# Kernel optimization log

Measured on AMD Instinct MI355X. Metric: run time of the kernel, lower is better.

The kernel has to match this reference:

```python
import jax, jax.numpy as jnp
import numpy as np

# Static per-expert capacities (tokens are laid out contiguously per expert)
CAPS = [1024, 512, 1024, 256, 1024, 512, 128, 1024, 512, 1024, 256, 512, 1024, 128, 64, 512]
TOTAL = sum(CAPS)  # 9536
E, H, I = 16, 1024, 4096
OFFSETS = np.concatenate([[0], np.cumsum(CAPS)])


def setup_inputs() -> dict:
    key = jax.random.key(0)
    ks = jax.random.split(key, 5)
    x = jax.random.normal(ks[0], (TOTAL, H), dtype=jnp.float32)
    W1 = jax.random.normal(ks[1], (E, I, H), dtype=jnp.float32) * 0.02
    b1 = jax.random.normal(ks[2], (E, I), dtype=jnp.float32) * 0.02
    W2 = jax.random.normal(ks[3], (E, H, I), dtype=jnp.float32) * 0.02
    b2 = jax.random.normal(ks[4], (E, H), dtype=jnp.float32) * 0.02
    return {"x": x, "W1": W1, "b1": b1, "W2": W2, "b2": b2}


def reference(x, W1, b1, W2, b2):
    # Grouped GEMM FFN: expert e processes rows [OFFSETS[e]:OFFSETS[e+1]]
    # out = gelu(x_e @ W1[e].T + b1[e]) @ W2[e].T + b2[e]
    outs = []
    for e in range(E):  # fixed, static loop over experts (capacities are static)
        xs = x[OFFSETS[e]:OFFSETS[e + 1]]                      # [cap_e, H]
        h = jax.nn.gelu(xs @ W1[e].T + b1[e], approximate=False)  # [cap_e, I]
        outs.append(h @ W2[e].T + b2[e])                       # [cap_e, H]
    return jnp.concatenate(outs, axis=0)                       # [TOTAL, H]
```

## Files before the change

### kernel.cpp

```cpp
#include <hip/hip_runtime.h>
#include <math.h>

typedef __attribute__((ext_vector_type(8))) short short8;
typedef __attribute__((ext_vector_type(4))) float f32x4;
typedef __attribute__((ext_vector_type(2))) unsigned int u32x2;
typedef __attribute__((ext_vector_type(4))) unsigned int u32x4;

#define E_NUM 16
constexpr int CAPS[E_NUM] = {1024,512,1024,256,1024,512,128,1024,512,1024,256,512,1024,128,64,512};
constexpr int OFFS[E_NUM] = {0,1024,1536,2560,2816,3840,4352,4480,5504,6016,7040,7296,7808,8832,8960,9024};
constexpr int cdiv_(int a, int b){ return (a + b - 1) / b; }
constexpr int ilog2_(int v){ int l = 0; while ((1 << l) < v) ++l; return l; }

__device__ __forceinline__ unsigned int cvt_pk_bf16(float a, float b){
  unsigned int r;
  asm("v_cvt_pk_bf16_f32 %0, %1, %2" : "=v"(r) : "v"(a), "v"(b));
  return r;
}

typedef __attribute__((address_space(1))) const unsigned char gas_u8;
typedef __attribute__((address_space(3))) unsigned char las_u8;
__device__ __forceinline__ void gl_lds16(const void* g, void* l){
  __builtin_amdgcn_global_load_lds((gas_u8*)g, (las_u8*)l, 16, 0, 0);
}

__global__ __launch_bounds__(256) void cvt_bf16_kernel(const float* __restrict__ x,
                                                       unsigned short* __restrict__ xb, int n8)
{
  int i = blockIdx.x * blockDim.x + threadIdx.x;
  const int stride = gridDim.x * blockDim.x;
  for (; i < n8; i += stride) {
    f32x4 a = *reinterpret_cast<const f32x4*>(x + (size_t)i * 8);
    f32x4 b = *reinterpret_cast<const f32x4*>(x + (size_t)i * 8 + 4);
    u32x2 lo, hi;
    lo[0] = cvt_pk_bf16(a[0], a[1]); lo[1] = cvt_pk_bf16(a[2], a[3]);
    hi[0] = cvt_pk_bf16(b[0], b[1]); hi[1] = cvt_pk_bf16(b[2], b[3]);
    *reinterpret_cast<u32x2*>(xb + (size_t)i * 8)     = lo;
    *reinterpret_cast<u32x2*>(xb + (size_t)i * 8 + 4) = hi;
  }
}

template<bool A_BF16, int NDIM, int KDIM, int LOG_GN, int NWG>
__global__ __launch_bounds__(512, 2)
void g1_gemm256(const void* __restrict__ Av, const float* __restrict__ W,
                const float* __restrict__ bias, void* __restrict__ Outv)
{
  constexpr int A_BYTES = 256 * 64;
  constexpr int B_BYTES = 256 * 128;
  constexpr int BUF  = A_BYTES + B_BYTES;
  constexpr int NBUF = A_BF16 ? 3 : 2;
  constexpr int GN   = 1 << LOG_GN;
  constexpr int NTT  = KDIM / 32;
  static_assert(NWG % 8 == 0);
  static_assert(NTT >= 3);

  __shared__ __align__(16) char smem[NBUF * BUF];

  const int tid  = threadIdx.x;
  const int braw = blockIdx.x;
  const int tt = (braw & 7) * (NWG / 8) + (braw >> 3);

  int m0 = 0, n0 = 0, Me = 0, tok0 = 0;
  size_t wbase = 0, bbase = 0;
  {
    int acc0 = 0;
    #pragma unroll
    for (int i = 0; i < E_NUM; ++i) {
      const int mt  = cdiv_(CAPS[i], 256);
      const int lmt = ilog2_(mt);
      const int nb  = mt * (NDIM / 256);
      if (tt >= acc0 && tt < acc0 + nb) {
        const int loc = tt - acc0;
        const int g   = loc >> (lmt + LOG_GN);
        const int rem = loc & ((mt << LOG_GN) - 1);
        m0   = (rem >> LOG_GN) * 256;
        n0   = ((g << LOG_GN) | (rem & (GN - 1))) * 256;
        Me   = CAPS[i];
        tok0 = OFFS[i];
        wbase = (size_t)i * NDIM * KDIM;
        bbase = (size_t)i * NDIM;
      }
      acc0 += nb;
    }
  }
  const float* Wb = W + wbase;

  const int lane = tid & 63;
  const int wv   = tid >> 6;

  const unsigned short* Ah = (const unsigned short*)Av;
  const float*          Af = (const float*)Av;

  auto stageA = [&](int buf, int kt) {
    const unsigned short* Ag = Ah + (size_t)(tok0 + m0) * KDIM + kt * 32;
    char* dst0 = smem + buf * BUF;
    #pragma unroll
    for (int j = 0; j < 2; ++j) {
      const int rbase = j * 128 + wv * 16;
      const int r     = rbase + (lane >> 2);
      const int blk   = (lane & 3) ^ (r & 3);
      gl_lds16((const void*)(Ag + (size_t)r * KDIM + blk * 8), (void*)(dst0 + rbase * 64));
    }
  };
  auto stageB = [&](int buf, int kt) {
    const float* Bg = Wb + (size_t)n0 * KDIM + kt * 32;
    char* dst0 = smem + buf * BUF + A_BYTES;
    #pragma unroll
    for (int j = 0; j < 4; ++j) {
      const int rbase = j * 64 + wv * 8;
      const int r     = rbase + (lane >> 3);
      const int blk   = (lane & 7) ^ (r & 7);
      gl_lds16((const void*)(Bg + (size_t)r * KDIM + blk * 4), (void*)(dst0 + rbase * 128));
    }
  };

  const int fr = tid >> 1;
  const int fcq = (tid & 1) * 2;
  f32x4 raf[4];
  auto loadA_reg = [&](int kt) {
    const float* Ap = Af + (size_t)(tok0 + m0 + fr) * KDIM + kt * 32 + fcq * 8;
    #pragma unroll
    for (int i = 0; i < 4; ++i) raf[i] = *reinterpret_cast<const f32x4*>(Ap + i * 4);
  };
  auto writeA_reg = [&](int buf) {
    char* ab = smem + buf * BUF;
    #pragma unroll
    for (int i = 0; i < 2; ++i) {
      u32x2 p;
      p[0] = cvt_pk_bf16(raf[2*i][0], raf[2*i][1]);
      p[1] = cvt_pk_bf16(raf[2*i][2], raf[2*i][3]);
      const int blk = (fcq + i) ^ (fr & 3);
      *reinterpret_cast<u32x2*>(ab + fr * 64 + blk * 16) = p;
    }
  };

  const int wm   = (wv >> 2) * 128;
  const int wn   = (wv & 3) * 64;
  const int lrow = lane & 15;
  const int pa0  = (((lane >> 4) ^ (lane & 3)) << 4);
  const int pb0  = ((((lane >> 4) << 1) ^ (lane & 7)) << 4);

  f32x4 acc_[8][4];
  #pragma unroll
  for (int i = 0; i < 8; ++i)
    #pragma unroll
    for (int j = 0; j < 4; ++j)
      acc_[i][j] = (f32x4){0.f, 0.f, 0.f, 0.f};

  auto compute = [&](int cur) {
    const char* ab  = smem + cur * BUF;
    const char* bbp = smem + cur * BUF + A_BYTES;
    short8 bfr[4];
    #pragma unroll
    for (int f = 0; f < 4; ++f) {
      const char* rowp = bbp + (size_t)(wn + f * 16 + lrow) * 128;
      f32x4 lo = *reinterpret_cast<const f32x4*>(rowp + pb0);
      f32x4 hi = *reinterpret_cast<const f32x4*>(rowp + (pb0 ^ 16));
      u32x4 pk;
      pk[0] = cvt_pk_bf16(lo[0], lo[1]); pk[1] = cvt_pk_bf16(lo[2], lo[3]);
      pk[2] = cvt_pk_bf16(hi[0], hi[1]); pk[3] = cvt_pk_bf16(hi[2], hi[3]);
      bfr[f] = __builtin_bit_cast(short8, pk);
    }
    #pragma unroll
    for (int i = 0; i < 8; ++i) {
      short8 afr = *reinterpret_cast<const short8*>(ab + (wm + i * 16 + lrow) * 64 + pa0);
      #pragma unroll
      for (int j = 0; j < 4; ++j)
        acc_[i][j] = __builtin_amdgcn_mfma_f32_16x16x32_bf16(afr, bfr[j], acc_[i][j], 0, 0, 0);
    }
  };

  if constexpr (A_BF16) {
    stageA(0, 0); stageB(0, 0);
    stageA(1, 1); stageB(1, 1);
    int cur = 0, nx2 = 2;
    for (int kt = 0; kt < NTT; ++kt) {
      if (kt + 1 < NTT) asm volatile("s_waitcnt vmcnt(6)\n\ts_barrier" ::: "memory");
      else              asm volatile("s_waitcnt vmcnt(0)\n\ts_barrier" ::: "memory");
      __builtin_amdgcn_sched_barrier(0);
      if (kt + 2 < NTT) { stageA(nx2, kt + 2); stageB(nx2, kt + 2); }
      compute(cur);
      cur = (cur == 2) ? 0 : cur + 1;
      nx2 = (nx2 == 2) ? 0 : nx2 + 1;
    }
  } else {
    loadA_reg(0); stageB(0, 0); writeA_reg(0);
    __syncthreads();
    for (int kt = 0; kt < NTT; ++kt) {
      const int cur = kt & 1;
      if (kt + 1 < NTT) { stageB(cur ^ 1, kt + 1); loadA_reg(kt + 1); }
      compute(cur);
      if (kt + 1 < NTT) writeA_reg(cur ^ 1);
      __syncthreads();
    }
  }

  float bv[4];
  #pragma unroll
  for (int f = 0; f < 4; ++f)
    bv[f] = bias[bbase + n0 + wn + f * 16 + lrow];

  unsigned short* Oh = (unsigned short*)Outv;
  if constexpr (A_BF16) {
    __syncthreads();
    unsigned short* hout = (unsigned short*)smem;
    #pragma unroll
    for (int i = 0; i < 8; ++i) {
      const int rbase = wm + i * 16 + (lane >> 4) * 4;
      #pragma unroll
      for (int j = 0; j < 4; ++j) {
        #pragma unroll
        for (int jj = 0; jj < 4; ++jj) {
          float xv = acc_[i][j][jj] + bv[j];
          float y2 = xv * (1.5957691216057308f + 0.07135481627f * xv * xv);
          float g  = xv * __builtin_amdgcn_rcpf(1.0f + __expf(-y2));
          hout[(rbase + jj) * 256 + wn + j * 16 + lrow] = (unsigned short)(cvt_pk_bf16(g, g) & 0xFFFFu);
        }
      }
    }
    __syncthreads();
    #pragma unroll
    for (int s = 0; s < 16; ++s) {
      const int row = s * 16 + (tid >> 5);
      const int c   = (tid & 31) * 8;
      if (m0 + row < Me) {
        *reinterpret_cast<short8*>(Oh + (size_t)(tok0 + m0 + row) * NDIM + n0 + c)
          = *reinterpret_cast<const short8*>(hout + row * 256 + c);
      }
    }
  } else {
    #pragma unroll
    for (int i = 0; i < 8; ++i) {
      const int rbase = wm + i * 16 + (lane >> 4) * 4;
      #pragma unroll
      for (int j = 0; j < 4; ++j) {
        #pragma unroll
        for (int jj = 0; jj < 4; ++jj) {
          int grow = m0 + rbase + jj;
          if (grow < Me) {
            float xv = acc_[i][j][jj] + bv[j];
            float y2 = xv * (1.5957691216057308f + 0.07135481627f * xv * xv);
            float g  = xv * __builtin_amdgcn_rcpf(1.0f + __expf(-y2));
            Oh[(size_t)(tok0 + grow) * NDIM + n0 + wn + j * 16 + lrow]
              = (unsigned short)(cvt_pk_bf16(g, g) & 0xFFFFu);
          }
        }
      }
    }
  }
}

template<int NDIM, int KDIM, int LOG_GN, int NWG, int KS>
__global__ __launch_bounds__(256, 8)
void g2_gemm128(const unsigned short* __restrict__ Ah, const float* __restrict__ W,
                const float* __restrict__ bias, float* __restrict__ Of)
{
  constexpr int A_BYTES = 128 * 64;
  constexpr int B_BYTES = 128 * 64;
  constexpr int GN   = 1 << LOG_GN;
  constexpr int NT   = KDIM / (KS * 32);
  constexpr int NWG1 = NWG / KS;
  static_assert(NWG % 8 == 0);

  __shared__ __align__(16) char smem[2 * A_BYTES + 2 * B_BYTES];

  const int tid  = threadIdx.x;
  const int braw = blockIdx.x;
  const int t = (braw & 7) * (NWG / 8) + (braw >> 3);

  const int kc    = t / NWG1;
  const int tt    = t % NWG1;
  const int kbase = kc * (KDIM / KS);

  int m0 = 0, n0 = 0, Me = 0, tok0 = 0;
  size_t wbase = 0, bbase = 0;
  {
    int acc0 = 0;
    #pragma unroll
    for (int i = 0; i < E_NUM; ++i) {
      const int mt  = cdiv_(CAPS[i], 128);
      const int lmt = ilog2_(mt);
      const int nb  = mt * (NDIM / 128);
      if (tt >= acc0 && tt < acc0 + nb) {
        const int loc = tt - acc0;
        const int g   = loc >> (lmt + LOG_GN);
        const int rem = loc & ((mt << LOG_GN) - 1);
        m0   = (rem >> LOG_GN) * 128;
        n0   = ((g << LOG_GN) | (rem & (GN - 1))) * 128;
        Me   = CAPS[i];
        tok0 = OFFS[i];
        wbase = (size_t)i * NDIM * KDIM;
        bbase = (size_t)i * NDIM;
      }
      acc0 += nb;
    }
  }
  const float* Wb = W + wbase;

  const int lane = tid & 63;
  const int wv   = tid >> 6;
  const int sr   = tid >> 3;
  const int sc   = (tid & 7) * 8;
  const int spc  = sc ^ (((sr >> 2) & 3) << 4);

  f32x4 rb[4];
  auto loadB = [&](int kt) {
    const int k0 = kbase + kt * 32;
    #pragma unroll
    for (int i = 0; i < 4; ++i)
      rb[i] = *reinterpret_cast<const f32x4*>(Wb + (size_t)(n0 + sr + 32 * i) * KDIM + k0 + (sc >> 1));
  };
  auto writeB = [&](int buf) {
    char* bb = smem + 2 * A_BYTES + buf * B_BYTES;
    #pragma unroll
    for (int i = 0; i < 4; ++i) {
      u32x2 p;
      p[0] = cvt_pk_bf16(rb[i][0], rb[i][1]);
      p[1] = cvt_pk_bf16(rb[i][2], rb[i][3]);
      *reinterpret_cast<u32x2*>(bb + (sr + 32 * i) * 64 + spc) = p;
    }
  };

  auto stageA = [&](int buf, int kt) {
    const unsigned short* Ag = Ah + (size_t)(tok0 + m0) * KDIM + kbase + kt * 32;
    char* dst0 = smem + buf * A_BYTES;
    #pragma unroll
    for (int j = 0; j < 2; ++j) {
      const int rbase = wv * 32 + j * 16;
      const int r     = rbase + (lane >> 2);
      const int blk   = (lane & 3) ^ ((r >> 2) & 3);
      gl_lds16((const void*)(Ag + (size_t)r * KDIM + blk * 8), (void*)(dst0 + rbase * 64));
    }
  };

  const int wm   = (wv >> 1) * 64;
  const int wn   = (wv & 1) * 64;
  const int lrow = lane & 15;
  const int fcs  = ((lane >> 4) << 4) ^ (((lane >> 2) & 3) << 4);

  f32x4 acc_[4][4];
  #pragma unroll
  for (int i = 0; i < 4; ++i)
    #pragma unroll
    for (int j = 0; j < 4; ++j)
      acc_[i][j] = (f32x4){0.f, 0.f, 0.f, 0.f};

  auto mfma_step = [&](int cur) {
    const char* ab = smem + cur * A_BYTES;
    const char* bb = smem + 2 * A_BYTES + cur * B_BYTES;
    short8 afr[4], bfr[4];
    #pragma unroll
    for (int f = 0; f < 4; ++f)
      afr[f] = *reinterpret_cast<const short8*>(ab + (wm + f * 16 + lrow) * 64 + fcs);
    #pragma unroll
    for (int f = 0; f < 4; ++f)
      bfr[f] = *reinterpret_cast<const short8*>(bb + (wn + f * 16 + lrow) * 64 + fcs);
    #pragma unroll
    for (int i = 0; i < 4; ++i)
      #pragma unroll
      for (int j = 0; j < 4; ++j)
        acc_[i][j] = __builtin_amdgcn_mfma_f32_16x16x32_bf16(afr[i], bfr[j], acc_[i][j], 0, 0, 0);
  };

  loadB(0); stageA(0, 0); writeB(0);
  __syncthreads();

  for (int kt = 0; kt < NT; ++kt) {
    const int cur = kt & 1;
    if (kt + 1 < NT) { loadB(kt + 1); stageA(cur ^ 1, kt + 1); }
    mfma_step(cur);
    if (kt + 1 < NT) writeB(cur ^ 1);
    __syncthreads();
  }

  float bv[4];
  #pragma unroll
  for (int f = 0; f < 4; ++f)
    bv[f] = bias[bbase + n0 + wn + f * 16 + lrow];

  constexpr float BS = 1.0f / (float)KS;
  #pragma unroll
  for (int i = 0; i < 4; ++i) {
    const int rbase = wm + i * 16 + (lane >> 4) * 4;
    #pragma unroll
    for (int jj = 0; jj < 4; ++jj) {
      int grow = m0 + rbase + jj;
      if (grow < Me) {
        #pragma unroll
        for (int j = 0; j < 4; ++j) {
          float v = acc_[i][j][jj] + bv[j] * BS;
          float* p = Of + (size_t)(tok0 + grow) * NDIM + n0 + wn + j * 16 + lrow;
          if constexpr (KS > 1) unsafeAtomicAdd(p, v);
          else                  *p = v;
        }
      }
    }
  }
}

extern "C" void kernel_launch(void* const* d_in, const int* in_sizes, int n_in,
                              void* d_out, int out_size, void* d_ws, size_t ws_size,
                              hipStream_t stream)
{
  const float* x  = (const float*)d_in[0];
  const float* W1 = (const float*)d_in[1];
  const float* b1 = (const float*)d_in[2];
  const float* W2 = (const float*)d_in[3];
  const float* b2 = (const float*)d_in[4];
  float* out = (float*)d_out;

  constexpr size_t H_BYTES  = (size_t)9536 * 4096 * 2;
  constexpr size_t XB_BYTES = (size_t)9536 * 1024 * 2;
  unsigned short* h  = (unsigned short*)d_ws;
  unsigned short* xb = (unsigned short*)((char*)d_ws + H_BYTES);

  const bool use_xb = ws_size >= H_BYTES + XB_BYTES;

  hipMemsetAsync(d_out, 0, (size_t)out_size * sizeof(float), stream);

  if (use_xb) {
    cvt_bf16_kernel<<<2048, 256, 0, stream>>>(x, xb, 9536 * 1024 / 8);
    g1_gemm256<true, 4096, 1024, 2, 624>
        <<<624, 512, 0, stream>>>((const void*)xb, W1, b1, (void*)h);
  } else {
    g1_gemm256<false, 4096, 1024, 2, 624>
        <<<624, 512, 0, stream>>>((const void*)x, W1, b1, (void*)h);
  }

  g2_gemm128<1024, 4096, 0, 1200, 2>
      <<<1200, 256, 0, stream>>>(h, W2, b2, out);
}
```

Baseline: 358.1 us.

## Load W2 fragments directly into registers and triple-buffer A in second GEMM

The second GEMM no longer stages the fp32 W2 tile through LDS. Each wave loads its own B fragments straight into registers, converts them to bf16 and feeds them to MFMA. The A tile (bf16 h) is triple-buffered through global_load_lds with explicit vmcnt waits and barriers, and the tile mapping drops the LOG_GN grouping. The aims are to cut LDS traffic and LDS size and to overlap loads better, at the cost of more registers (launch bounds drop from 8 to 3) and redundant global B loads, since both wave rows re-read the same W2 columns.

New measurement: 521.7 us. 45.7% more time.

```diff
diff --git a/kernel.cpp b/kernel.cpp
--- a/kernel.cpp
+++ b/kernel.cpp
@@ -250,19 +250,18 @@
   }
 }
 
-template<int NDIM, int KDIM, int LOG_GN, int NWG, int KS>
-__global__ __launch_bounds__(256, 8)
+template<int NDIM, int KDIM, int NWG, int KS>
+__global__ __launch_bounds__(256, 3)
 void g2_gemm128(const unsigned short* __restrict__ Ah, const float* __restrict__ W,
                 const float* __restrict__ bias, float* __restrict__ Of)
 {
   constexpr int A_BYTES = 128 * 64;
-  constexpr int B_BYTES = 128 * 64;
-  constexpr int GN   = 1 << LOG_GN;
   constexpr int NT   = KDIM / (KS * 32);
   constexpr int NWG1 = NWG / KS;
   static_assert(NWG % 8 == 0);
-
-  __shared__ __align__(16) char smem[2 * A_BYTES + 2 * B_BYTES];
+  static_assert(NT >= 4 && (NT % 2) == 0);
+
+  __shared__ __align__(16) char smem[3 * A_BYTES];
 
   const int tid  = threadIdx.x;
   const int braw = blockIdx.x;
@@ -279,14 +278,11 @@
     #pragma unroll
     for (int i = 0; i < E_NUM; ++i) {
       const int mt  = cdiv_(CAPS[i], 128);
-      const int lmt = ilog2_(mt);
       const int nb  = mt * (NDIM / 128);
       if (tt >= acc0 && tt < acc0 + nb) {
         const int loc = tt - acc0;
-        const int g   = loc >> (lmt + LOG_GN);
-        const int rem = loc & ((mt << LOG_GN) - 1);
-        m0   = (rem >> LOG_GN) * 128;
-        n0   = ((g << LOG_GN) | (rem & (GN - 1))) * 128;
+        m0   = (loc & (mt - 1)) * 128;
+        n0   = (loc >> ilog2_(mt)) * 128;
         Me   = CAPS[i];
         tok0 = OFFS[i];
         wbase = (size_t)i * NDIM * KDIM;
@@ -299,44 +295,31 @@
 
   const int lane = tid & 63;
   const int wv   = tid >> 6;
-  const int sr   = tid >> 3;
-  const int sc   = (tid & 7) * 8;
-  const int spc  = sc ^ (((sr >> 2) & 3) << 4);
-
-  f32x4 rb[4];
-  auto loadB = [&](int kt) {
-    const int k0 = kbase + kt * 32;
-    #pragma unroll
-    for (int i = 0; i < 4; ++i)
-      rb[i] = *reinterpret_cast<const f32x4*>(Wb + (size_t)(n0 + sr + 32 * i) * KDIM + k0 + (sc >> 1));
-  };
-  auto writeB = [&](int buf) {
-    char* bb = smem + 2 * A_BYTES + buf * B_BYTES;
-    #pragma unroll
-    for (int i = 0; i < 4; ++i) {
-      u32x2 p;
-      p[0] = cvt_pk_bf16(rb[i][0], rb[i][1]);
-      p[1] = cvt_pk_bf16(rb[i][2], rb[i][3]);
-      *reinterpret_cast<u32x2*>(bb + (sr + 32 * i) * 64 + spc) = p;
-    }
-  };
-
-  auto stageA = [&](int buf, int kt) {
+  const int wm   = (wv >> 1) * 64;
+  const int wn   = (wv & 1) * 64;
+  const int lrow = lane & 15;
+  const int pa0  = (((lane >> 4) ^ (lane & 3)) << 4);
+
+  auto stageA = [&](char* dst0, int kt) {
     const unsigned short* Ag = Ah + (size_t)(tok0 + m0) * KDIM + kbase + kt * 32;
-    char* dst0 = smem + buf * A_BYTES;
     #pragma unroll
     for (int j = 0; j < 2; ++j) {
       const int rbase = wv * 32 + j * 16;
       const int r     = rbase + (lane >> 2);
-      const int blk   = (lane & 3) ^ ((r >> 2) & 3);
+      const int blk   = (lane & 3) ^ (r & 3);
       gl_lds16((const void*)(Ag + (size_t)r * KDIM + blk * 8), (void*)(dst0 + rbase * 64));
     }
   };
 
-  const int wm   = (wv >> 1) * 64;
-  const int wn   = (wv & 1) * 64;
-  const int lrow = lane & 15;
-  const int fcs  = ((lane >> 4) << 4) ^ (((lane >> 2) & 3) << 4);
+  const float* Bbase = Wb + (size_t)(n0 + wn + lrow) * KDIM + kbase + (lane >> 4) * 8;
+  auto loadB = [&](f32x4 (&R)[8], int kt) {
+    const float* p = Bbase + kt * 32;
+    #pragma unroll
+    for (int f = 0; f < 4; ++f) {
+      R[2*f]     = *reinterpret_cast<const f32x4*>(p + (size_t)f * 16 * KDIM);
+      R[2*f + 1] = *reinterpret_cast<const f32x4*>(p + (size_t)f * 16 * KDIM + 4);
+    }
+  };
 
   f32x4 acc_[4][4];
   #pragma unroll
@@ -345,16 +328,20 @@
     for (int j = 0; j < 4; ++j)
       acc_[i][j] = (f32x4){0.f, 0.f, 0.f, 0.f};
 
-  auto mfma_step = [&](int cur) {
-    const char* ab = smem + cur * A_BYTES;
-    const char* bb = smem + 2 * A_BYTES + cur * B_BYTES;
+  auto compute = [&](const char* ab, f32x4 (&BR)[8]) {
     short8 afr[4], bfr[4];
     #pragma unroll
+    for (int f = 0; f < 4; ++f) {
+      u32x4 pk;
+      pk[0] = cvt_pk_bf16(BR[2*f][0],   BR[2*f][1]);
+      pk[1] = cvt_pk_bf16(BR[2*f][2],   BR[2*f][3]);
+      pk[2] = cvt_pk_bf16(BR[2*f+1][0], BR[2*f+1][1]);
+      pk[3] = cvt_pk_bf16(BR[2*f+1][2], BR[2*f+1][3]);
+      bfr[f] = __builtin_bit_cast(short8, pk);
+    }
+    #pragma unroll
     for (int f = 0; f < 4; ++f)
-      afr[f] = *reinterpret_cast<const short8*>(ab + (wm + f * 16 + lrow) * 64 + fcs);
-    #pragma unroll
-    for (int f = 0; f < 4; ++f)
-      bfr[f] = *reinterpret_cast<const short8*>(bb + (wn + f * 16 + lrow) * 64 + fcs);
+      afr[f] = *reinterpret_cast<const short8*>(ab + (wm + f * 16 + lrow) * 64 + pa0);
     #pragma unroll
     for (int i = 0; i < 4; ++i)
       #pragma unroll
@@ -362,15 +349,23 @@
         acc_[i][j] = __builtin_amdgcn_mfma_f32_16x16x32_bf16(afr[i], bfr[j], acc_[i][j], 0, 0, 0);
   };
 
-  loadB(0); stageA(0, 0); writeB(0);
-  __syncthreads();
-
-  for (int kt = 0; kt < NT; ++kt) {
-    const int cur = kt & 1;
-    if (kt + 1 < NT) { loadB(kt + 1); stageA(cur ^ 1, kt + 1); }
-    mfma_step(cur);
-    if (kt + 1 < NT) writeB(cur ^ 1);
-    __syncthreads();
+  f32x4 B0[8], B1[8];
+  stageA(smem + 0 * A_BYTES, 0);
+  stageA(smem + 1 * A_BYTES, 1);
+  loadB(B0, 0);
+
+  for (int kt = 0; kt < NT; kt += 2) {
+    asm volatile("s_waitcnt vmcnt(10)\n\ts_barrier" ::: "memory");
+    __builtin_amdgcn_sched_barrier(0);
+    loadB(B1, kt + 1);
+    if (kt + 2 < NT) stageA(smem + ((kt + 2) % 3) * A_BYTES, kt + 2);
+    compute(smem + (kt % 3) * A_BYTES, B0);
+    if (kt + 2 < NT) asm volatile("s_waitcnt vmcnt(10)\n\ts_barrier" ::: "memory");
+    else             asm volatile("s_waitcnt vmcnt(8)\n\ts_barrier"  ::: "memory");
+    __builtin_amdgcn_sched_barrier(0);
+    if (kt + 2 < NT) loadB(B0, kt + 2);
+    if (kt + 3 < NT) stageA(smem + ((kt + 3) % 3) * A_BYTES, kt + 3);
+    compute(smem + ((kt + 1) % 3) * A_BYTES, B1);
   }
 
   float bv[4];
@@ -427,6 +422,6 @@
         <<<624, 512, 0, stream>>>((const void*)x, W1, b1, (void*)h);
   }
 
-  g2_gemm128<1024, 4096, 0, 1200, 2>
+  g2_gemm128<1024, 4096, 1200, 2>
       <<<1200, 256, 0, stream>>>(h, W2, b2, out);
 }
```

## Pre-convert W2 to bf16 and triple-buffer direct-to-LDS loads in second GEMM

Applied to the files above, without the earlier changes.

Adds a pass that converts W2 from fp32 to bf16 in workspace, provided the workspace is large enough. The second GEMM can then stage both A and B tiles with direct global-to-LDS loads through a three-stage ring buffer, using explicit vmcnt waits and barriers in place of register staging with a full sync each step. It also simplifies tile ordering and changes the LDS swizzle. The trade is an extra full read and write of W2 (about 256MB fp32) on every call, plus lower occupancy from the launch bounds of 3.

New measurement: 377.1 us. 5.3% more time.

```diff
diff --git a/kernel.cpp b/kernel.cpp
--- a/kernel.cpp
+++ b/kernel.cpp
@@ -250,19 +250,18 @@
   }
 }
 
-template<int NDIM, int KDIM, int LOG_GN, int NWG, int KS>
-__global__ __launch_bounds__(256, 8)
-void g2_gemm128(const unsigned short* __restrict__ Ah, const float* __restrict__ W,
+template<bool B_BF16, int NDIM, int KDIM, int NWG, int KS>
+__global__ __launch_bounds__(256, 3)
+void g2_gemm128(const unsigned short* __restrict__ Ah, const void* __restrict__ Wv,
                 const float* __restrict__ bias, float* __restrict__ Of)
 {
-  constexpr int A_BYTES = 128 * 64;
-  constexpr int B_BYTES = 128 * 64;
-  constexpr int GN   = 1 << LOG_GN;
+  constexpr int AB_BYTES = 128 * 64;
   constexpr int NT   = KDIM / (KS * 32);
   constexpr int NWG1 = NWG / KS;
   static_assert(NWG % 8 == 0);
-
-  __shared__ __align__(16) char smem[2 * A_BYTES + 2 * B_BYTES];
+  static_assert(NT >= 3);
+
+  __shared__ __align__(16) char smem[B_BF16 ? 6 * AB_BYTES : 4 * AB_BYTES];
 
   const int tid  = threadIdx.x;
   const int braw = blockIdx.x;
@@ -279,14 +278,11 @@
     #pragma unroll
     for (int i = 0; i < E_NUM; ++i) {
       const int mt  = cdiv_(CAPS[i], 128);
-      const int lmt = ilog2_(mt);
       const int nb  = mt * (NDIM / 128);
       if (tt >= acc0 && tt < acc0 + nb) {
         const int loc = tt - acc0;
-        const int g   = loc >> (lmt + LOG_GN);
-        const int rem = loc & ((mt << LOG_GN) - 1);
-        m0   = (rem >> LOG_GN) * 128;
-        n0   = ((g << LOG_GN) | (rem & (GN - 1))) * 128;
+        m0   = (loc & (mt - 1)) * 128;
+        n0   = (loc >> ilog2_(mt)) * 128;
         Me   = CAPS[i];
         tok0 = OFFS[i];
         wbase = (size_t)i * NDIM * KDIM;
@@ -295,48 +291,24 @@
       acc0 += nb;
     }
   }
-  const float* Wb = W + wbase;
 
   const int lane = tid & 63;
   const int wv   = tid >> 6;
-  const int sr   = tid >> 3;
-  const int sc   = (tid & 7) * 8;
-  const int spc  = sc ^ (((sr >> 2) & 3) << 4);
-
-  f32x4 rb[4];
-  auto loadB = [&](int kt) {
-    const int k0 = kbase + kt * 32;
-    #pragma unroll
-    for (int i = 0; i < 4; ++i)
-      rb[i] = *reinterpret_cast<const f32x4*>(Wb + (size_t)(n0 + sr + 32 * i) * KDIM + k0 + (sc >> 1));
-  };
-  auto writeB = [&](int buf) {
-    char* bb = smem + 2 * A_BYTES + buf * B_BYTES;
-    #pragma unroll
-    for (int i = 0; i < 4; ++i) {
-      u32x2 p;
-      p[0] = cvt_pk_bf16(rb[i][0], rb[i][1]);
-      p[1] = cvt_pk_bf16(rb[i][2], rb[i][3]);
-      *reinterpret_cast<u32x2*>(bb + (sr + 32 * i) * 64 + spc) = p;
-    }
-  };
-
-  auto stageA = [&](int buf, int kt) {
-    const unsigned short* Ag = Ah + (size_t)(tok0 + m0) * KDIM + kbase + kt * 32;
-    char* dst0 = smem + buf * A_BYTES;
+  const int wm   = (wv >> 1) * 64;
+  const int wn   = (wv & 1) * 64;
+  const int lrow = lane & 15;
+  const int pa0  = (((lane >> 4) ^ (lane & 3)) << 4);
+
+  auto stage_bf16 = [&](const unsigned short* base, char* dst0, int kt) {
+    const unsigned short* Tg = base + kt * 32;
     #pragma unroll
     for (int j = 0; j < 2; ++j) {
       const int rbase = wv * 32 + j * 16;
       const int r     = rbase + (lane >> 2);
-      const int blk   = (lane & 3) ^ ((r >> 2) & 3);
-      gl_lds16((const void*)(Ag + (size_t)r * KDIM + blk * 8), (void*)(dst0 + rbase * 64));
-    }
-  };
-
-  const int wm   = (wv >> 1) * 64;
-  const int wn   = (wv & 1) * 64;
-  const int lrow = lane & 15;
-  const int fcs  = ((lane >> 4) << 4) ^ (((lane >> 2) & 3) << 4);
+      const int blk   = (lane & 3) ^ (r & 3);
+      gl_lds16((const void*)(Tg + (size_t)r * KDIM + blk * 8), (void*)(dst0 + rbase * 64));
+    }
+  };
 
   f32x4 acc_[4][4];
   #pragma unroll
@@ -345,16 +317,14 @@
     for (int j = 0; j < 4; ++j)
       acc_[i][j] = (f32x4){0.f, 0.f, 0.f, 0.f};
 
-  auto mfma_step = [&](int cur) {
-    const char* ab = smem + cur * A_BYTES;
-    const char* bb = smem + 2 * A_BYTES + cur * B_BYTES;
+  auto mfma_ab = [&](const char* ab, const char* bb) {
     short8 afr[4], bfr[4];
     #pragma unroll
     for (int f = 0; f < 4; ++f)
-      afr[f] = *reinterpret_cast<const short8*>(ab + (wm + f * 16 + lrow) * 64 + fcs);
+      afr[f] = *reinterpret_cast<const short8*>(ab + (wm + f * 16 + lrow) * 64 + pa0);
     #pragma unroll
     for (int f = 0; f < 4; ++f)
-      bfr[f] = *reinterpret_cast<const short8*>(bb + (wn + f * 16 + lrow) * 64 + fcs);
+      bfr[f] = *reinterpret_cast<const short8*>(bb + (wn + f * 16 + lrow) * 64 + pa0);
     #pragma unroll
     for (int i = 0; i < 4; ++i)
       #pragma unroll
@@ -362,15 +332,88 @@
         acc_[i][j] = __builtin_amdgcn_mfma_f32_16x16x32_bf16(afr[i], bfr[j], acc_[i][j], 0, 0, 0);
   };
 
-  loadB(0); stageA(0, 0); writeB(0);
-  __syncthreads();
-
-  for (int kt = 0; kt < NT; ++kt) {
-    const int cur = kt & 1;
-    if (kt + 1 < NT) { loadB(kt + 1); stageA(cur ^ 1, kt + 1); }
-    mfma_step(cur);
-    if (kt + 1 < NT) writeB(cur ^ 1);
+  const unsigned short* Abase = Ah + (size_t)(tok0 + m0) * KDIM + kbase;
+
+  if constexpr (B_BF16) {
+    const unsigned short* Wh = (const unsigned short*)Wv;
+    const unsigned short* Bbase = Wh + wbase + (size_t)n0 * KDIM + kbase;
+    auto stage = [&](int buf, int kt) {
+      stage_bf16(Abase, smem + buf * 2 * AB_BYTES, kt);
+      stage_bf16(Bbase, smem + buf * 2 * AB_BYTES + AB_BYTES, kt);
+    };
+    stage(0, 0);
+    stage(1, 1);
+    int cur = 0, nx2 = 2;
+    for (int kt = 0; kt < NT; ++kt) {
+      if (kt + 1 < NT) asm volatile("s_waitcnt vmcnt(4)\n\ts_barrier" ::: "memory");
+      else             asm volatile("s_waitcnt vmcnt(0)\n\ts_barrier" ::: "memory");
+      __builtin_amdgcn_sched_barrier(0);
+      if (kt + 2 < NT) stage(nx2, kt + 2);
+      mfma_ab(smem + cur * 2 * AB_BYTES, smem + cur * 2 * AB_BYTES + AB_BYTES);
+      cur = (cur == 2) ? 0 : cur + 1;
+      nx2 = (nx2 == 2) ? 0 : nx2 + 1;
+    }
+  } else {
+    const float* Wb = (const float*)Wv + wbase;
+    const int sr  = tid >> 3;
+    const int sc  = (tid & 7) * 8;
+    const int spc = sc ^ (((sr >> 2) & 3) << 4);
+    const int fcs = ((lane >> 4) << 4) ^ (((lane >> 2) & 3) << 4);
+    char* asm_ = smem;
+    char* bsm_ = smem + 2 * AB_BYTES;
+    f32x4 rb[4];
+    auto loadB = [&](int kt) {
+      const int k0 = kbase + kt * 32;
+      #pragma unroll
+      for (int i = 0; i < 4; ++i)
+        rb[i] = *reinterpret_cast<const f32x4*>(Wb + (size_t)(n0 + sr + 32 * i) * KDIM + k0 + (sc >> 1));
+    };
+    auto writeB = [&](int buf) {
+      char* bb = bsm_ + buf * AB_BYTES;
+      #pragma unroll
+      for (int i = 0; i < 4; ++i) {
+        u32x2 p;
+        p[0] = cvt_pk_bf16(rb[i][0], rb[i][1]);
+        p[1] = cvt_pk_bf16(rb[i][2], rb[i][3]);
+        *reinterpret_cast<u32x2*>(bb + (sr + 32 * i) * 64 + spc) = p;
+      }
+    };
+    auto stageA2 = [&](int buf, int kt) {
+      char* dst0 = asm_ + buf * AB_BYTES;
+      const unsigned short* Tg = Abase + kt * 32;
+      #pragma unroll
+      for (int j = 0; j < 2; ++j) {
+        const int rbase = wv * 32 + j * 16;
+        const int r     = rbase + (lane >> 2);
+        const int blk   = (lane & 3) ^ ((r >> 2) & 3);
+        gl_lds16((const void*)(Tg + (size_t)r * KDIM + blk * 8), (void*)(dst0 + rbase * 64));
+      }
+    };
+    auto mfma2 = [&](int cur) {
+      const char* ab = asm_ + cur * AB_BYTES;
+      const char* bb = bsm_ + cur * AB_BYTES;
+      short8 afr[4], bfr[4];
+      #pragma unroll
+      for (int f = 0; f < 4; ++f)
+        afr[f] = *reinterpret_cast<const short8*>(ab + (wm + f * 16 + lrow) * 64 + fcs);
+      #pragma unroll
+      for (int f = 0; f < 4; ++f)
+        bfr[f] = *reinterpret_cast<const short8*>(bb + (wn + f * 16 + lrow) * 64 + fcs);
+      #pragma unroll
+      for (int i = 0; i < 4; ++i)
+        #pragma unroll
+        for (int j = 0; j < 4; ++j)
+          acc_[i][j] = __builtin_amdgcn_mfma_f32_16x16x32_bf16(afr[i], bfr[j], acc_[i][j], 0, 0, 0);
+    };
+    loadB(0); stageA2(0, 0); writeB(0);
     __syncthreads();
+    for (int kt = 0; kt < NT; ++kt) {
+      const int cur = kt & 1;
+      if (kt + 1 < NT) { loadB(kt + 1); stageA2(cur ^ 1, kt + 1); }
+      mfma2(cur);
+      if (kt + 1 < NT) writeB(cur ^ 1);
+      __syncthreads();
+    }
   }
 
   float bv[4];
@@ -409,14 +452,20 @@
   const float* b2 = (const float*)d_in[4];
   float* out = (float*)d_out;
 
-  constexpr size_t H_BYTES  = (size_t)9536 * 4096 * 2;
-  constexpr size_t XB_BYTES = (size_t)9536 * 1024 * 2;
-  unsigned short* h  = (unsigned short*)d_ws;
-  unsigned short* xb = (unsigned short*)((char*)d_ws + H_BYTES);
-
-  const bool use_xb = ws_size >= H_BYTES + XB_BYTES;
+  constexpr size_t H_BYTES   = (size_t)9536 * 4096 * 2;
+  constexpr size_t XB_BYTES  = (size_t)9536 * 1024 * 2;
+  constexpr size_t W2B_BYTES = (size_t)16 * 1024 * 4096 * 2;
+  unsigned short* h   = (unsigned short*)d_ws;
+  unsigned short* xb  = (unsigned short*)((char*)d_ws + H_BYTES);
+  unsigned short* w2b = (unsigned short*)((char*)d_ws + H_BYTES + XB_BYTES);
+
+  const bool use_xb  = ws_size >= H_BYTES + XB_BYTES;
+  const bool use_w2b = ws_size >= H_BYTES + XB_BYTES + W2B_BYTES;
 
   hipMemsetAsync(d_out, 0, (size_t)out_size * sizeof(float), stream);
+
+  if (use_w2b)
+    cvt_bf16_kernel<<<2048, 256, 0, stream>>>(W2, w2b, 16 * 1024 * 4096 / 8);
 
   if (use_xb) {
     cvt_bf16_kernel<<<2048, 256, 0, stream>>>(x, xb, 9536 * 1024 / 8);
@@ -427,6 +476,11 @@
         <<<624, 512, 0, stream>>>((const void*)x, W1, b1, (void*)h);
   }
 
-  g2_gemm128<1024, 4096, 0, 1200, 2>
-      <<<1200, 256, 0, stream>>>(h, W2, b2, out);
-}
+  if (use_w2b) {
+    g2_gemm128<true, 1024, 4096, 1200, 2>
+        <<<1200, 256, 0, stream>>>(h, (const void*)w2b, b2, out);
+  } else {
+    g2_gemm128<false, 1024, 4096, 1200, 2>
+        <<<1200, 256, 0, stream>>>(h, (const void*)W2, b2, out);
+  }
+}
```
